# Kernel tuning notes

Measured on AMD Instinct MI355X. Metric: run time of the kernel, lower is better.

Reference implementation:

```python
import jax, jax.numpy as jnp
import numpy as np

N = 50000        # nodes
DEG = 16         # fixed out-degree per row (CSR)
E = N * DEG      # edges
H = 4            # attention heads
D = 32           # head feature dim
NEG_SLOPE = 0.2  # GAT leaky-relu slope (scalar hyperparam from forward args)


def setup_inputs() -> dict:
    key = jax.random.key(0)
    k1, k2, k3, k4 = jax.random.split(key, 4)
    attn_row = jax.random.normal(k1, (N, H), dtype=jnp.float32)   # a_dst . Wh_i per head
    attn_col = jax.random.normal(k2, (N, H), dtype=jnp.float32)   # a_src . Wh_j per head
    in_feat = jax.random.normal(k3, (N, H, D), dtype=jnp.float32)  # transformed node feats
    col_indices = jax.random.randint(k4, (E,), 0, N, dtype=jnp.int32)
    row_indptr = (jnp.arange(N + 1, dtype=jnp.int32) * DEG)        # CSR pointers, fixed degree
    return {
        "attn_row": attn_row,
        "attn_col": attn_col,
        "in_feat": in_feat,
        "row_indptr": row_indptr,
        "col_indices": col_indices,
    }


def reference(attn_row, attn_col, in_feat, row_indptr, col_indices):
    # Fused GAT: per-edge score = leaky_relu(attn_row[i] + attn_col[j]),
    # softmax over each destination row's edges, then weighted sparse aggregation.
    n = attn_row.shape[0]
    e = col_indices.shape[0]
    # row id of each edge from CSR indptr (jit-safe, static edge count)
    row_ids = jnp.searchsorted(row_indptr, jnp.arange(e, dtype=row_indptr.dtype), side="right") - 1
    score = jax.nn.leaky_relu(attn_row[row_ids] + attn_col[col_indices], NEG_SLOPE)  # [E,H]
    # numerically-stable edge softmax per destination row
    m = jax.ops.segment_max(score, row_ids, num_segments=n)        # [N,H]
    ex = jnp.exp(score - m[row_ids])                               # [E,H]
    denom = jax.ops.segment_sum(ex, row_ids, num_segments=n)       # [N,H]
    alpha = ex / denom[row_ids]                                    # [E,H]
    # gather neighbor features, weight, scatter-add to destinations
    msg = alpha[:, :, None] * in_feat[col_indices]                 # [E,H,D]
    out = jax.ops.segment_sum(msg, row_ids, num_segments=n)        # [N,H,D]
    return out
```

## Files before the change

kernel.cpp:

```cpp
#include <hip/hip_runtime.h>
#include <math.h>


#define GAT_H 4
#define GAT_D 32
#define GAT_DEG 16
#define GAT_NEG_SLOPE 0.2f

__global__ __launch_bounds__(256, 4) void gat_fused_kernel(
    const float* __restrict__ attn_row,
    const float* __restrict__ attn_col,
    const float* __restrict__ in_feat,
    const int*   __restrict__ row_indptr,
    const int*   __restrict__ col_indices,
    float*       __restrict__ out,
    int n)
{
    const int wave_id = (int)((blockIdx.x * (unsigned)blockDim.x + threadIdx.x) >> 6);
    const int lane    = threadIdx.x & 63;
    if (wave_id >= n) return;
    const int i = wave_id;

    const int start = row_indptr[i];
    const int deg   = row_indptr[i + 1] - start;

    const int e = lane & 15;
    const int h = lane >> 4;

    float s    = -INFINITY;
    int   colv = 0;
    if (e < deg) {
        colv = col_indices[start + e];
        const float ar = attn_row[i * GAT_H + h];
        const float ac = attn_col[colv * GAT_H + h];
        const float x  = ar + ac;
        s = (x > 0.0f) ? x : GAT_NEG_SLOPE * x;
    }

    float m = s;
    #pragma unroll
    for (int off = 1; off < 16; off <<= 1)
        m = fmaxf(m, __shfl_xor(m, off));

    float ex = (e < deg) ? __expf(s - m) : 0.0f;

    float denom = ex;
    #pragma unroll
    for (int off = 1; off < 16; off <<= 1)
        denom += __shfl_xor(denom, off);

    const float alpha = ex / denom;

    const int d0   = (lane & 15) * 2;
    const int base = lane & 48;

    float accx = 0.0f, accy = 0.0f;
    #pragma unroll
    for (int k = 0; k < GAT_DEG; ++k) {
        const int   idx = __shfl(colv,  base + k);
        const float a   = __shfl(alpha, base + k);
        const float2 f  = *reinterpret_cast<const float2*>(
            &in_feat[((long)idx * GAT_H + h) * GAT_D + d0]);
        accx = fmaf(a, f.x, accx);
        accy = fmaf(a, f.y, accy);
    }

    *reinterpret_cast<float2*>(&out[((long)i * GAT_H + h) * GAT_D + d0]) =
        make_float2(accx, accy);
}

extern "C" void kernel_launch(void* const* d_in, const int* in_sizes, int n_in,
                              void* d_out, int out_size, void* d_ws, size_t ws_size,
                              hipStream_t stream) {
    const float* attn_row    = (const float*)d_in[0];
    const float* attn_col    = (const float*)d_in[1];
    const float* in_feat     = (const float*)d_in[2];
    const int*   row_indptr  = (const int*)d_in[3];
    const int*   col_indices = (const int*)d_in[4];
    float*       out         = (float*)d_out;

    const int n = in_sizes[0] / GAT_H;

    const int threads = 256;
    const int nodes_per_block = threads / 64;
    const int blocks = (n + nodes_per_block - 1) / nodes_per_block;

    gat_fused_kernel<<<blocks, threads, 0, stream>>>(
        attn_row, attn_col, in_feat, row_indptr, col_indices, out, n);
}
```

Baseline: 135.2 us.

## Convert features to head-major fp16 and map heads to XCDs for L2 locality

Adds a pre-pass that converts in_feat to fp16 in a head-major layout in the workspace. The main kernel assigns each block to one head, with head chosen from the block's XCD index, so each XCD's L2 only caches one head's slice of the feature table. Softmax normalization is deferred to a single reciprocal multiply at the end. The fp16 path loses precision in the aggregated features and adds a full read and write of in_feat each call, which may or may not pay off against the halved and more cache-local gathers.

```diff
diff --git a/kernel.cpp b/kernel.cpp
--- a/kernel.cpp
+++ b/kernel.cpp
@@ -1,4 +1,5 @@
 #include <hip/hip_runtime.h>
+#include <hip/hip_fp16.h>
 #include <math.h>
 
 
@@ -7,33 +8,52 @@
 #define GAT_DEG 16
 #define GAT_NEG_SLOPE 0.2f
 
-__global__ __launch_bounds__(256, 4) void gat_fused_kernel(
-    const float* __restrict__ attn_row,
-    const float* __restrict__ attn_col,
-    const float* __restrict__ in_feat,
-    const int*   __restrict__ row_indptr,
-    const int*   __restrict__ col_indices,
-    float*       __restrict__ out,
-    int n)
+__global__ __launch_bounds__(256) void gat_cvt_kernel(
+    const float* __restrict__ in, __half2* __restrict__ outp, int n )
 {
-    const int wave_id = (int)((blockIdx.x * (unsigned)blockDim.x + threadIdx.x) >> 6);
-    const int lane    = threadIdx.x & 63;
-    if (wave_id >= n) return;
-    const int i = wave_id;
+    const int p = blockIdx.x * blockDim.x + threadIdx.x;
+    const int npairs = n * GAT_H * (GAT_D / 2);
+    if (p < npairs) {
+        const int c  = p & 15;
+        const int h  = (p >> 4) & 3;
+        const int nn = p >> 6;
+        const float2 v = reinterpret_cast<const float2*>(in)[p];
+        outp[((size_t)h * n + nn) * (GAT_D / 2) + c] = __floats2half2_rn(v.x, v.y);
+    }
+}
 
-    const int start = row_indptr[i];
-    const int deg   = row_indptr[i + 1] - start;
+template <bool FP16>
+__global__ __launch_bounds__(256, 4) void gat_main_kernel(
+    const float*   __restrict__ attn_row,
+    const float*   __restrict__ attn_col,
+    const float*   __restrict__ in_feat,
+    const __half2* __restrict__ feat16,
+    const int*     __restrict__ row_indptr,
+    const int*     __restrict__ col_indices,
+    float*         __restrict__ out,
+    int n, int nb )
+{
+    const int b   = blockIdx.x;
+    const int xcd = b & 7;
+    const int h   = xcd >> 1;
+    const int j   = (b >> 3) * 2 + (xcd & 1);
+    if (j >= nb) return;
 
-    const int e = lane & 15;
-    const int h = lane >> 4;
+    const int lane = threadIdx.x & 63;
+    const int wid  = threadIdx.x >> 6;
+    const int g    = lane >> 4;
+    const int e    = lane & 15;
+    const int dst  = j * 16 + wid * 4 + g;
+    if (dst >= n) return;
 
+    const int start = row_indptr[dst];
+    const int deg   = row_indptr[dst + 1] - start;
+
+    int   colv = 0;
     float s    = -INFINITY;
-    int   colv = 0;
     if (e < deg) {
         colv = col_indices[start + e];
-        const float ar = attn_row[i * GAT_H + h];
-        const float ac = attn_col[colv * GAT_H + h];
-        const float x  = ar + ac;
+        const float x = attn_row[dst * GAT_H + h] + attn_col[colv * GAT_H + h];
         s = (x > 0.0f) ? x : GAT_NEG_SLOPE * x;
     }
 
@@ -42,31 +62,36 @@
     for (int off = 1; off < 16; off <<= 1)
         m = fmaxf(m, __shfl_xor(m, off));
 
-    float ex = (e < deg) ? __expf(s - m) : 0.0f;
+    const float ex = (e < deg) ? __expf(s - m) : 0.0f;
 
     float denom = ex;
     #pragma unroll
     for (int off = 1; off < 16; off <<= 1)
         denom += __shfl_xor(denom, off);
 
-    const float alpha = ex / denom;
+    const float alpha  = ex;
+    const float rdenom = __builtin_amdgcn_rcpf(denom);
 
-    const int d0   = (lane & 15) * 2;
     const int base = lane & 48;
-
     float accx = 0.0f, accy = 0.0f;
     #pragma unroll
     for (int k = 0; k < GAT_DEG; ++k) {
-        const int   idx = __shfl(colv,  base + k);
+        const int   src = __shfl(colv,  base + k);
         const float a   = __shfl(alpha, base + k);
-        const float2 f  = *reinterpret_cast<const float2*>(
-            &in_feat[((long)idx * GAT_H + h) * GAT_D + d0]);
+        float2 f;
+        if (FP16) {
+            const __half2 hv = feat16[((size_t)h * n + src) * (GAT_D / 2) + e];
+            f = __half22float2(hv);
+        } else {
+            f = *reinterpret_cast<const float2*>(
+                &in_feat[((size_t)src * GAT_H + h) * GAT_D + e * 2]);
+        }
         accx = fmaf(a, f.x, accx);
         accy = fmaf(a, f.y, accy);
     }
 
-    *reinterpret_cast<float2*>(&out[((long)i * GAT_H + h) * GAT_D + d0]) =
-        make_float2(accx, accy);
+    reinterpret_cast<float2*>(out)[((size_t)dst * GAT_H + h) * (GAT_D / 2) + e] =
+        make_float2(accx * rdenom, accy * rdenom);
 }
 
 extern "C" void kernel_launch(void* const* d_in, const int* in_sizes, int n_in,
@@ -79,12 +104,24 @@
     const int*   col_indices = (const int*)d_in[4];
     float*       out         = (float*)d_out;
 
-    const int n = in_sizes[0] / GAT_H;
+    const int n      = in_sizes[0] / GAT_H;
+    const int n_feat = in_sizes[2];
 
-    const int threads = 256;
-    const int nodes_per_block = threads / 64;
-    const int blocks = (n + nodes_per_block - 1) / nodes_per_block;
+    const int nb = (n + 15) / 16;
+    const int kmax   = (nb + 1) / 2;
+    const int blocks = kmax * 8;
 
-    gat_fused_kernel<<<blocks, threads, 0, stream>>>(
-        attn_row, attn_col, in_feat, row_indptr, col_indices, out, n);
+    const size_t fp16_bytes = (size_t)n_feat * sizeof(__half);
+    if (ws_size >= fp16_bytes) {
+        __half2* feat_h = (__half2*)d_ws;
+        const int npairs = n_feat / 2;
+        gat_cvt_kernel<<<(npairs + 255) / 256, 256, 0, stream>>>(in_feat, feat_h, n);
+        gat_main_kernel<true><<<blocks, 256, 0, stream>>>(
+            attn_row, attn_col, in_feat, feat_h, row_indptr, col_indices,
+            out, n, nb);
+    } else {
+        gat_main_kernel<false><<<blocks, 256, 0, stream>>>(
+            attn_row, attn_col, in_feat, (const __half2*)nullptr,
+            row_indptr, col_indices, out, n, nb);
+    }
 }
```

After: 122.1 us. -9.7%, faster.
